# Optimization experiments

Measured on AMD Instinct MI355X. Metric: run time of the kernel, lower is better.

The kernel has to match this reference:

```python
import jax, jax.numpy as jnp
import numpy as np

SEQ_LEN = 8192
DIM_AUD = 2048
NEG_SLOPE = 0.02


def _leaky(z):
    return jnp.where(z >= 0, z, NEG_SLOPE * z)


def _conv1d(x, w, b):
    # x: [1, Cin, L], w: [Cout, Cin, 3], b: [Cout]; stride 1, padding 1
    y = jax.lax.conv_general_dilated(
        x, w, window_strides=(1,), padding=[(1, 1)],
        dimension_numbers=('NCH', 'OIH', 'NCH'))
    return y + b[None, :, None]


def setup_inputs() -> dict:
    key = jax.random.key(0)
    ks = jax.random.split(key, 13)
    def rn(k, shape, fan_in):
        return jax.random.normal(k, shape, dtype=jnp.float32) * (1.0 / np.sqrt(fan_in))
    x = jax.random.normal(ks[0], (SEQ_LEN, DIM_AUD), dtype=jnp.float32)
    w1 = rn(ks[1], (16, DIM_AUD, 3), DIM_AUD * 3); b1 = jnp.zeros((16,), jnp.float32)
    w2 = rn(ks[2], (8, 16, 3), 16 * 3);            b2 = jnp.zeros((8,), jnp.float32)
    w3 = rn(ks[3], (4, 8, 3), 8 * 3);              b3 = jnp.zeros((4,), jnp.float32)
    w4 = rn(ks[4], (2, 4, 3), 4 * 3);              b4 = jnp.zeros((2,), jnp.float32)
    w5 = rn(ks[5], (1, 2, 3), 2 * 3);              b5 = jnp.zeros((1,), jnp.float32)
    Wl = rn(ks[6], (SEQ_LEN, SEQ_LEN), SEQ_LEN);   bl = jnp.zeros((SEQ_LEN,), jnp.float32)
    return {"x": x, "w1": w1, "b1": b1, "w2": w2, "b2": b2, "w3": w3, "b3": b3,
            "w4": w4, "b4": b4, "w5": w5, "b5": b5, "Wl": Wl, "bl": bl}


def reference(x, w1, b1, w2, b2, w3, b3, w4, b4, w5, b5, Wl, bl):
    # y: [1, dim_aud, seq_len]
    y = x[:, :DIM_AUD].T[None]
    y = _leaky(_conv1d(y, w1, b1))
    y = _leaky(_conv1d(y, w2, b2))
    y = _leaky(_conv1d(y, w3, b3))
    y = _leaky(_conv1d(y, w4, b4))
    y = _leaky(_conv1d(y, w5, b5))          # [1, 1, seq_len]
    logits = y.reshape(1, SEQ_LEN) @ Wl.T + bl  # torch Linear: x @ W.T + b
    att = jax.nn.softmax(logits, axis=1).reshape(SEQ_LEN, 1)
    return jnp.sum(att * x, axis=0)          # [dim_aud]
```

## Files before the change

### kernel.cpp

```cpp
#include <hip/hip_runtime.h>

#define SEQ 8192
#define DIM 2048
#define NEG 0.02f

typedef short bf16x8 __attribute__((ext_vector_type(8)));
typedef float f32x4 __attribute__((ext_vector_type(4)));

__device__ __forceinline__ unsigned short bf16_rne(float f, float* as_f32) {
  unsigned u = __float_as_uint(f);
  unsigned r = (u + 0x7FFFu + ((u >> 16) & 1u)) >> 16;
  *as_f32 = __uint_as_float(r << 16);
  return (unsigned short)r;
}

__global__ __launch_bounds__(256) void k_prep_wA(
    const float* __restrict__ w1, unsigned short* __restrict__ wA) {
  int e = blockIdx.x * 256 + threadIdx.x;
  int lane = e & 63;
  int g = e >> 6;
  int p = g & 1; g >>= 1;
  int ks = g & 3; g >>= 2;
  int ko = g % 3; g /= 3;
  int ch = g & 3;
  int sl = g >> 2;
  int c = lane & 15;
  unsigned short* dst = wA + (size_t)e * 8;
  #pragma unroll
  for (int j = 0; j < 8; ++j) {
    int kk = ((lane >> 4) << 3) + j;
    int cin = sl * 512 + ch * 128 + ks * 32 + kk;
    float w = w1[c * 6144 + cin * 3 + ko];
    float hf;
    unsigned short hb = bf16_rne(w, &hf);
    if (p == 0) dst[j] = hb;
    else {
      float lf;
      dst[j] = bf16_rne(w - hf, &lf);
    }
  }
}

__global__ __launch_bounds__(256, 2) void k_conv1(
    const float* __restrict__ x, const unsigned short* __restrict__ wA,
    float* __restrict__ out1p) {
  __shared__ char xsh[66 * 256];
  __shared__ char xsl[66 * 256];

  const int tid = threadIdx.x;
  const int tb = blockIdx.x & 127;
  const int sl = blockIdx.x >> 7;
  const int t0 = tb << 6;
  const int lane = tid & 63;
  const int wv = tid >> 6;
  const float4* x4 = (const float4*)x;

  const int xcol = sl * 128 + (tid & 31);
  const int cq8 = (tid & 31) * 8;
  const int r0s = tid >> 5;

  f32x4 acc = {0.f, 0.f, 0.f, 0.f};

  for (int ch = 0; ch < 4; ++ch) {
    __syncthreads();
    #pragma unroll
    for (int pp = 0; pp < 9; ++pp) {
      int r = r0s + pp * 8;
      if (r < 66) {
        int gt = t0 - 1 + r;
        float4 v = make_float4(0.f, 0.f, 0.f, 0.f);
        if (gt >= 0 && gt < SEQ) v = x4[gt * 512 + ch * 32 + xcol];
        float h0f, h1f, h2f, h3f, d;
        ushort4 hv, lv;
        hv.x = bf16_rne(v.x, &h0f); lv.x = bf16_rne(v.x - h0f, &d);
        hv.y = bf16_rne(v.y, &h1f); lv.y = bf16_rne(v.y - h1f, &d);
        hv.z = bf16_rne(v.z, &h2f); lv.z = bf16_rne(v.z - h2f, &d);
        hv.w = bf16_rne(v.w, &h3f); lv.w = bf16_rne(v.w - h3f, &d);
        int off = r * 256 + (cq8 ^ ((r & 7) << 4));
        *(ushort4*)(xsh + off) = hv;
        *(ushort4*)(xsl + off) = lv;
      }
    }
    __syncthreads();

    #pragma unroll
    for (int ko = 0; ko < 3; ++ko) {
      const int lr = (wv << 4) + (lane & 15) + ko;
      const int rowb = lr * 256;
      const int sw = (lr & 7) << 4;
      #pragma unroll
      for (int ks = 0; ks < 4; ++ks) {
        int ebase = (((((sl * 4 + ch) * 3 + ko) * 4 + ks) * 2) << 6) + lane;
        bf16x8 Ah = *(const bf16x8*)(wA + (size_t)ebase * 8);
        bf16x8 Al = *(const bf16x8*)(wA + (size_t)(ebase + 64) * 8);
        int cb = ((ks << 6) + ((lane >> 4) << 4)) ^ sw;
        bf16x8 Bh = *(const bf16x8*)(xsh + rowb + cb);
        bf16x8 Bl = *(const bf16x8*)(xsl + rowb + cb);
        acc = __builtin_amdgcn_mfma_f32_16x16x32_bf16(Ah, Bh, acc, 0, 0, 0);
        acc = __builtin_amdgcn_mfma_f32_16x16x32_bf16(Ah, Bl, acc, 0, 0, 0);
        acc = __builtin_amdgcn_mfma_f32_16x16x32_bf16(Al, Bh, acc, 0, 0, 0);
      }
    }
  }

  const int t = t0 + (wv << 4) + (lane & 15);
  const int c0 = (lane >> 4) << 2;
  #pragma unroll
  for (int i = 0; i < 4; ++i)
    out1p[(sl * 16 + c0 + i) * SEQ + t] = acc[i];
}

__global__ __launch_bounds__(128) void k_chain(
    const float* __restrict__ out1p, const float* __restrict__ b1,
    const float* __restrict__ w2, const float* __restrict__ b2,
    const float* __restrict__ w3, const float* __restrict__ b3,
    const float* __restrict__ w4, const float* __restrict__ b4,
    const float* __restrict__ w5, const float* __restrict__ b5,
    float* __restrict__ y5) {
  __shared__ float l1[16][72], l2[8][72], l3[4][72], l4[2][72];
  __shared__ float w2s[384], w3s[96], w4s[24], w5s[6];
  __shared__ float bs[16];

  const int tid = threadIdx.x;
  const int t0 = blockIdx.x * 64;

  for (int i = tid; i < 384; i += 128) w2s[i] = w2[i];
  if (tid < 96) w3s[tid] = w3[tid];
  else if (tid < 120) w4s[tid - 96] = w4[tid - 96];
  else if (tid == 120) { for (int i = 0; i < 6; ++i) w5s[i] = w5[i]; }
  else if (tid == 121) {
    for (int i = 0; i < 8; ++i) bs[i] = b2[i];
    for (int i = 0; i < 4; ++i) bs[8 + i] = b3[i];
    bs[12] = b4[0]; bs[13] = b4[1]; bs[14] = b5[0];
  }

  const float4* p4 = (const float4*)out1p;
  for (int idx = tid; idx < 16 * 18; idx += 128) {
    int cc = idx / 18, m = idx - cc * 18;
    int gt0 = t0 - 4 + 4 * m;
    if (gt0 >= 0 && gt0 < SEQ) {
      float4 a = make_float4(0.f, 0.f, 0.f, 0.f);
      int base = cc * 2048 + (gt0 >> 2);
      #pragma unroll
      for (int s = 0; s < 4; ++s) {
        float4 v = p4[s * 16 * 2048 + base];
        a.x += v.x; a.y += v.y; a.z += v.z; a.w += v.w;
      }
      float bb = b1[cc];
      float e0 = a.x + bb, e1 = a.y + bb, e2 = a.z + bb, e3 = a.w + bb;
      l1[cc][4 * m + 0] = (e0 >= 0.f) ? e0 : NEG * e0;
      l1[cc][4 * m + 1] = (e1 >= 0.f) ? e1 : NEG * e1;
      l1[cc][4 * m + 2] = (e2 >= 0.f) ? e2 : NEG * e2;
      l1[cc][4 * m + 3] = (e3 >= 0.f) ? e3 : NEG * e3;
    } else {
      l1[cc][4 * m + 0] = 0.f; l1[cc][4 * m + 1] = 0.f;
      l1[cc][4 * m + 2] = 0.f; l1[cc][4 * m + 3] = 0.f;
    }
  }
  __syncthreads();

  for (int o = tid; o < 560; o += 128) {
    int j = (o >> 3) + 1, cc = o & 7;
    float acc = bs[cc];
    #pragma unroll
    for (int ci = 0; ci < 16; ++ci) {
      acc += w2s[cc * 48 + ci * 3 + 0] * l1[ci][j - 1];
      acc += w2s[cc * 48 + ci * 3 + 1] * l1[ci][j];
      acc += w2s[cc * 48 + ci * 3 + 2] * l1[ci][j + 1];
    }
    l2[cc][j] = (acc >= 0.f) ? acc : NEG * acc;
  }
  __syncthreads();

  for (int o = tid; o < 272; o += 128) {
    int j = (o >> 2) + 2, cc = o & 3;
    float acc = bs[8 + cc];
    #pragma unroll
    for (int ci = 0; ci < 8; ++ci) {
      acc += w3s[cc * 24 + ci * 3 + 0] * l2[ci][j - 1];
      acc += w3s[cc * 24 + ci * 3 + 1] * l2[ci][j];
      acc += w3s[cc * 24 + ci * 3 + 2] * l2[ci][j + 1];
    }
    l3[cc][j] = (acc >= 0.f) ? acc : NEG * acc;
  }
  __syncthreads();

  for (int o = tid; o < 132; o += 128) {
    int j = (o >> 1) + 3, cc = o & 1;
    float acc = bs[12 + cc];
    #pragma unroll
    for (int ci = 0; ci < 4; ++ci) {
      acc += w4s[cc * 12 + ci * 3 + 0] * l3[ci][j - 1];
      acc += w4s[cc * 12 + ci * 3 + 1] * l3[ci][j];
      acc += w4s[cc * 12 + ci * 3 + 2] * l3[ci][j + 1];
    }
    l4[cc][j] = (acc >= 0.f) ? acc : NEG * acc;
  }
  __syncthreads();

  for (int o = tid; o < 64; o += 128) {
    int j = o + 4;
    float acc = bs[14];
    #pragma unroll
    for (int ci = 0; ci < 2; ++ci) {
      acc += w5s[ci * 3 + 0] * l4[ci][j - 1];
      acc += w5s[ci * 3 + 1] * l4[ci][j];
      acc += w5s[ci * 3 + 2] * l4[ci][j + 1];
    }
    y5[t0 + o] = (acc >= 0.f) ? acc : NEG * acc;
  }
}

__global__ __launch_bounds__(256) void k_matvec(
    const float* __restrict__ Wl, const float* __restrict__ bl,
    const float* __restrict__ y5, float* __restrict__ logits) {
  const int tid = threadIdx.x;
  const int r0 = blockIdx.x * 8;
  const float4* W4 = (const float4*)Wl;
  const float4* y4 = (const float4*)y5;

  float a[8];
  #pragma unroll
  for (int r = 0; r < 8; ++r) a[r] = 0.f;

  #pragma unroll 2
  for (int u = 0; u < 8; ++u) {
    int i = u * 256 + tid;
    float4 yv = y4[i];
    #pragma unroll
    for (int r = 0; r < 8; ++r) {
      float4 wv = W4[(r0 + r) * 2048 + i];
      a[r] += wv.x * yv.x + wv.y * yv.y + wv.z * yv.z + wv.w * yv.w;
    }
  }
  #pragma unroll
  for (int o = 32; o; o >>= 1) {
    #pragma unroll
    for (int r = 0; r < 8; ++r) a[r] += __shfl_down(a[r], o);
  }
  __shared__ float red[4][8];
  const int lane = tid & 63, wid = tid >> 6;
  if (lane == 0) {
    #pragma unroll
    for (int r = 0; r < 8; ++r) red[wid][r] = a[r];
  }
  __syncthreads();
  if (tid < 8) {
    float s = red[0][tid] + red[1][tid] + red[2][tid] + red[3][tid];
    logits[r0 + tid] = s + bl[r0 + tid];
  }
}

__global__ __launch_bounds__(256) void k_stats(
    const float* __restrict__ logits, float* __restrict__ stats) {
  __shared__ float red[4];
  const int tid = threadIdx.x;
  const int lane = tid & 63, wid = tid >> 6;

  float lv[32];
  #pragma unroll
  for (int i = 0; i < 32; ++i) lv[i] = logits[tid + 256 * i];

  float m = lv[0];
  #pragma unroll
  for (int i = 1; i < 32; ++i) m = fmaxf(m, lv[i]);
  #pragma unroll
  for (int o = 32; o; o >>= 1) m = fmaxf(m, __shfl_down(m, o));
  if (lane == 0) red[wid] = m;
  __syncthreads();
  const float M = fmaxf(fmaxf(red[0], red[1]), fmaxf(red[2], red[3]));
  __syncthreads();

  float s = 0.f;
  #pragma unroll
  for (int i = 0; i < 32; ++i) s += __expf(lv[i] - M);
  #pragma unroll
  for (int o = 32; o; o >>= 1) s += __shfl_down(s, o);
  if (lane == 0) red[wid] = s;
  __syncthreads();
  if (tid == 0) {
    float S = red[0] + red[1] + red[2] + red[3];
    stats[0] = M;
    stats[1] = 1.0f / S;
  }
}

__global__ __launch_bounds__(256) void k_wsum(
    const float* __restrict__ x, const float* __restrict__ logits,
    const float* __restrict__ stats, float* __restrict__ partial) {
  const int tid = threadIdx.x;
  const int lane = tid & 63, wv = tid >> 6;
  const int tc = blockIdx.x >> 3, strip = blockIdx.x & 7;
  const float M = stats[0], invS = stats[1];
  const float4* x4 = (const float4*)x;
  const int col = strip * 64 + lane;
  const int t0 = tc * 64 + wv * 16;

  float4 acc = make_float4(0.f, 0.f, 0.f, 0.f);
  #pragma unroll 4
  for (int tt = 0; tt < 16; ++tt) {
    int t = t0 + tt;
    float a = __expf(logits[t] - M) * invS;
    float4 xv = x4[t * 512 + col];
    acc.x += a * xv.x; acc.y += a * xv.y; acc.z += a * xv.z; acc.w += a * xv.w;
  }

  __shared__ float4 redx[4][64];
  redx[wv][lane] = acc;
  __syncthreads();
  if (wv == 0) {
    float4 s = redx[0][lane];
    #pragma unroll
    for (int w = 1; w < 4; ++w) {
      float4 v = redx[w][lane];
      s.x += v.x; s.y += v.y; s.z += v.z; s.w += v.w;
    }
    ((float4*)partial)[tc * 512 + col] = s;
  }
}

__global__ __launch_bounds__(256) void k_reduce(
    const float* __restrict__ partial, float* __restrict__ out) {
  const int col = blockIdx.x * 256 + threadIdx.x;
  float s = 0.f;
  #pragma unroll 8
  for (int tc = 0; tc < 128; ++tc) s += partial[tc * 2048 + col];
  out[col] = s;
}

extern "C" void kernel_launch(void* const* d_in, const int* in_sizes, int n_in,
                              void* d_out, int out_size, void* d_ws, size_t ws_size,
                              hipStream_t stream) {
  const float* x  = (const float*)d_in[0];
  const float* w1 = (const float*)d_in[1];
  const float* b1 = (const float*)d_in[2];
  const float* w2 = (const float*)d_in[3];
  const float* b2 = (const float*)d_in[4];
  const float* w3 = (const float*)d_in[5];
  const float* b3 = (const float*)d_in[6];
  const float* w4 = (const float*)d_in[7];
  const float* b4 = (const float*)d_in[8];
  const float* w5 = (const float*)d_in[9];
  const float* b5 = (const float*)d_in[10];
  const float* Wl = (const float*)d_in[11];
  const float* bl = (const float*)d_in[12];
  float* out = (float*)d_out;

  float* ws      = (float*)d_ws;
  unsigned short* wA = (unsigned short*)ws;
  float* out1p   = ws + 98304;
  float* y5      = out1p + 4 * 16 * SEQ;
  float* logits  = y5 + SEQ;
  float* stats   = logits + SEQ;
  float* partial = stats + 16;

  k_prep_wA<<<96, 256, 0, stream>>>(w1, wA);
  k_conv1  <<<512, 256, 0, stream>>>(x, wA, out1p);
  k_chain  <<<128, 128, 0, stream>>>(out1p, b1, w2, b2, w3, b3, w4, b4, w5, b5, y5);
  k_matvec <<<1024, 256, 0, stream>>>(Wl, bl, y5, logits);
  k_stats  <<<1, 256, 0, stream>>>(logits, stats);
  k_wsum   <<<1024, 256, 0, stream>>>(x, logits, stats, partial);
  k_reduce <<<8, 256, 0, stream>>>(partial, out);
}
```

Before: 106.0 us.

## Prefetch conv1 input chunks into registers and fuse softmax stats into weighted sum

The conv1 kernel now loads the next channel chunk of x into registers while the MFMA work for the current chunk runs, so global-load latency overlaps with compute. The matvec kernel loads its y5 vector slice into registers once, before the loop. The single-block softmax-stats kernel is removed: each wsum block computes a local max and sum-of-exps for its time chunk, and the final reduce rescales the partials with an online-softmax combine. This drops one serialized single-block launch at the cost of extra registers and a small rescale in the reduce.

```diff
diff --git a/kernel.cpp b/kernel.cpp
--- a/kernel.cpp
+++ b/kernel.cpp
@@ -60,6 +60,16 @@
   const int r0s = tid >> 5;
 
   f32x4 acc = {0.f, 0.f, 0.f, 0.f};
+  float4 xreg[9];
+
+  #pragma unroll
+  for (int pp = 0; pp < 9; ++pp) {
+    int r = r0s + pp * 8;
+    int gt = t0 - 1 + r;
+    float4 v = make_float4(0.f, 0.f, 0.f, 0.f);
+    if (r < 66 && gt >= 0 && gt < SEQ) v = x4[gt * 512 + xcol];
+    xreg[pp] = v;
+  }
 
   for (int ch = 0; ch < 4; ++ch) {
     __syncthreads();
@@ -67,9 +77,7 @@
     for (int pp = 0; pp < 9; ++pp) {
       int r = r0s + pp * 8;
       if (r < 66) {
-        int gt = t0 - 1 + r;
-        float4 v = make_float4(0.f, 0.f, 0.f, 0.f);
-        if (gt >= 0 && gt < SEQ) v = x4[gt * 512 + ch * 32 + xcol];
+        float4 v = xreg[pp];
         float h0f, h1f, h2f, h3f, d;
         ushort4 hv, lv;
         hv.x = bf16_rne(v.x, &h0f); lv.x = bf16_rne(v.x - h0f, &d);
@@ -82,6 +90,18 @@
       }
     }
     __syncthreads();
+
+    if (ch < 3) {
+      #pragma unroll
+      for (int pp = 0; pp < 9; ++pp) {
+        int r = r0s + pp * 8;
+        int gt = t0 - 1 + r;
+        float4 v = make_float4(0.f, 0.f, 0.f, 0.f);
+        if (r < 66 && gt >= 0 && gt < SEQ)
+          v = x4[gt * 512 + (ch + 1) * 32 + xcol];
+        xreg[pp] = v;
+      }
+    }
 
     #pragma unroll
     for (int ko = 0; ko < 3; ++ko) {
@@ -219,6 +239,10 @@
   const float4* W4 = (const float4*)Wl;
   const float4* y4 = (const float4*)y5;
 
+  float4 yv[8];
+  #pragma unroll
+  for (int u = 0; u < 8; ++u) yv[u] = y4[u * 256 + tid];
+
   float a[8];
   #pragma unroll
   for (int r = 0; r < 8; ++r) a[r] = 0.f;
@@ -226,11 +250,10 @@
   #pragma unroll 2
   for (int u = 0; u < 8; ++u) {
     int i = u * 256 + tid;
-    float4 yv = y4[i];
     #pragma unroll
     for (int r = 0; r < 8; ++r) {
       float4 wv = W4[(r0 + r) * 2048 + i];
-      a[r] += wv.x * yv.x + wv.y * yv.y + wv.z * yv.z + wv.w * yv.w;
+      a[r] += wv.x * yv[u].x + wv.y * yv[u].y + wv.z * yv[u].z + wv.w * yv[u].w;
     }
   }
   #pragma unroll
@@ -251,81 +274,87 @@
   }
 }
 
-__global__ __launch_bounds__(256) void k_stats(
-    const float* __restrict__ logits, float* __restrict__ stats) {
-  __shared__ float red[4];
-  const int tid = threadIdx.x;
-  const int lane = tid & 63, wid = tid >> 6;
-
-  float lv[32];
-  #pragma unroll
-  for (int i = 0; i < 32; ++i) lv[i] = logits[tid + 256 * i];
-
-  float m = lv[0];
-  #pragma unroll
-  for (int i = 1; i < 32; ++i) m = fmaxf(m, lv[i]);
-  #pragma unroll
-  for (int o = 32; o; o >>= 1) m = fmaxf(m, __shfl_down(m, o));
-  if (lane == 0) red[wid] = m;
-  __syncthreads();
-  const float M = fmaxf(fmaxf(red[0], red[1]), fmaxf(red[2], red[3]));
-  __syncthreads();
-
-  float s = 0.f;
-  #pragma unroll
-  for (int i = 0; i < 32; ++i) s += __expf(lv[i] - M);
-  #pragma unroll
-  for (int o = 32; o; o >>= 1) s += __shfl_down(s, o);
-  if (lane == 0) red[wid] = s;
-  __syncthreads();
-  if (tid == 0) {
-    float S = red[0] + red[1] + red[2] + red[3];
-    stats[0] = M;
-    stats[1] = 1.0f / S;
-  }
-}
-
 __global__ __launch_bounds__(256) void k_wsum(
     const float* __restrict__ x, const float* __restrict__ logits,
-    const float* __restrict__ stats, float* __restrict__ partial) {
+    float* __restrict__ partial, float* __restrict__ ms) {
   const int tid = threadIdx.x;
   const int lane = tid & 63, wv = tid >> 6;
   const int tc = blockIdx.x >> 3, strip = blockIdx.x & 7;
-  const float M = stats[0], invS = stats[1];
+  const int t0 = tc * 64 + wv * 16;
+  __shared__ float wm[4], wssum[4];
+
+  float lv[16];
+  #pragma unroll
+  for (int tt = 0; tt < 16; ++tt) lv[tt] = logits[t0 + tt];
+  float m = lv[0];
+  #pragma unroll
+  for (int tt = 1; tt < 16; ++tt) m = fmaxf(m, lv[tt]);
+  if (lane == 0) wm[wv] = m;
+  __syncthreads();
+  const float mb = fmaxf(fmaxf(wm[0], wm[1]), fmaxf(wm[2], wm[3]));
+
+  float av[16];
+  float s = 0.f;
+  #pragma unroll
+  for (int tt = 0; tt < 16; ++tt) { av[tt] = __expf(lv[tt] - mb); s += av[tt]; }
+  if (lane == 0) wssum[wv] = s;
+  __syncthreads();
+  if (strip == 0 && tid == 0) {
+    ms[2 * tc] = mb;
+    ms[2 * tc + 1] = wssum[0] + wssum[1] + wssum[2] + wssum[3];
+  }
+
   const float4* x4 = (const float4*)x;
   const int col = strip * 64 + lane;
-  const int t0 = tc * 64 + wv * 16;
-
   float4 acc = make_float4(0.f, 0.f, 0.f, 0.f);
   #pragma unroll 4
   for (int tt = 0; tt < 16; ++tt) {
-    int t = t0 + tt;
-    float a = __expf(logits[t] - M) * invS;
-    float4 xv = x4[t * 512 + col];
-    acc.x += a * xv.x; acc.y += a * xv.y; acc.z += a * xv.z; acc.w += a * xv.w;
+    float4 xv = x4[(t0 + tt) * 512 + col];
+    acc.x += av[tt] * xv.x; acc.y += av[tt] * xv.y;
+    acc.z += av[tt] * xv.z; acc.w += av[tt] * xv.w;
   }
 
   __shared__ float4 redx[4][64];
   redx[wv][lane] = acc;
   __syncthreads();
   if (wv == 0) {
-    float4 s = redx[0][lane];
+    float4 sx = redx[0][lane];
     #pragma unroll
     for (int w = 1; w < 4; ++w) {
       float4 v = redx[w][lane];
-      s.x += v.x; s.y += v.y; s.z += v.z; s.w += v.w;
-    }
-    ((float4*)partial)[tc * 512 + col] = s;
+      sx.x += v.x; sx.y += v.y; sx.z += v.z; sx.w += v.w;
+    }
+    ((float4*)partial)[tc * 512 + col] = sx;
   }
 }
 
 __global__ __launch_bounds__(256) void k_reduce(
-    const float* __restrict__ partial, float* __restrict__ out) {
-  const int col = blockIdx.x * 256 + threadIdx.x;
-  float s = 0.f;
+    const float* __restrict__ ms, const float* __restrict__ partial,
+    float* __restrict__ out) {
+  __shared__ float mv[128], sv[128], fac[128];
+  __shared__ float sMI[2];
+  const int tid = threadIdx.x;
+
+  if (tid < 128) { mv[tid] = ms[2 * tid]; sv[tid] = ms[2 * tid + 1]; }
+  __syncthreads();
+  if (tid == 0) {
+    float M = mv[0];
+    for (int i = 1; i < 128; ++i) M = fmaxf(M, mv[i]);
+    float S = 0.f;
+    for (int i = 0; i < 128; ++i) S += sv[i] * __expf(mv[i] - M);
+    sMI[0] = M;
+    sMI[1] = 1.0f / S;
+  }
+  __syncthreads();
+  if (tid < 128) fac[tid] = __expf(mv[tid] - sMI[0]);
+  __syncthreads();
+
+  const float invS = sMI[1];
+  const int col = blockIdx.x * 256 + tid;
+  float acc = 0.f;
   #pragma unroll 8
-  for (int tc = 0; tc < 128; ++tc) s += partial[tc * 2048 + col];
-  out[col] = s;
+  for (int tc = 0; tc < 128; ++tc) acc += fac[tc] * partial[tc * 2048 + col];
+  out[col] = acc * invS;
 }
 
 extern "C" void kernel_launch(void* const* d_in, const int* in_sizes, int n_in,
@@ -351,14 +380,13 @@
   float* out1p   = ws + 98304;
   float* y5      = out1p + 4 * 16 * SEQ;
   float* logits  = y5 + SEQ;
-  float* stats   = logits + SEQ;
-  float* partial = stats + 16;
+  float* ms      = logits + SEQ;
+  float* partial = ms + 256;
 
   k_prep_wA<<<96, 256, 0, stream>>>(w1, wA);
   k_conv1  <<<512, 256, 0, stream>>>(x, wA, out1p);
   k_chain  <<<128, 128, 0, stream>>>(out1p, b1, w2, b2, w3, b3, w4, b4, w5, b5, y5);
   k_matvec <<<1024, 256, 0, stream>>>(Wl, bl, y5, logits);
-  k_stats  <<<1, 256, 0, stream>>>(logits, stats);
-  k_wsum   <<<1024, 256, 0, stream>>>(x, logits, stats, partial);
-  k_reduce <<<8, 256, 0, stream>>>(partial, out);
-}
+  k_wsum   <<<1024, 256, 0, stream>>>(x, logits, partial, ms);
+  k_reduce <<<8, 256, 0, stream>>>(ms, partial, out);
+}
```

New measurement: 132.6 us. 1.25x slower.
